# Optimization experiments

Measured on AMD Instinct MI355X. Metric: run time of the kernel, lower is better.

Reference implementation:

```python
import jax, jax.numpy as jnp
import numpy as np

EPS_STAB = 1e-9   # numerical_stabilizer default
BN_EPS = 1e-5     # flax BatchNorm default epsilon


def setup_inputs() -> dict:
    key = jax.random.key(0)
    ks = jax.random.split(key, 5)
    B, N, C = 2, 4096, 512
    s = 1.0 / np.sqrt(C)
    d = {"inputs": jax.random.normal(ks[0], (B, N, C), jnp.float32)}
    # 1x1 convs == pointwise linear maps [C_in, C_out] + bias
    for i, w in enumerate(["Wq", "Wk", "Wv", "Wo"]):
        d[w] = jax.random.normal(ks[1 + i], (C, C), jnp.float32) * s
    for b in ["bq", "bk", "bv", "bo"]:
        d[b] = jnp.zeros((C,), jnp.float32)
    # BatchNorm (inference: use_running_average=True since train=False)
    d["bn_scale"] = jnp.ones((C,), jnp.float32)
    d["bn_bias"] = jnp.zeros((C,), jnp.float32)
    d["bn_mean"] = jnp.zeros((C,), jnp.float32)
    d["bn_var"] = jnp.ones((C,), jnp.float32)
    return d


def reference(inputs, Wq, bq, Wk, bk, Wv, bv, Wo, bo,
              bn_scale, bn_bias, bn_mean, bn_var):
    # QKV via 1x1 conv == dense projection. [B, N, C]
    q = inputs @ Wq + bq
    k = inputs @ Wk + bk
    v = inputs @ Wv + bv
    # scores [B, M, N]; softmax over last axis (N)
    att = jax.nn.softmax(jnp.einsum('bmc,bnc->bmn', q, k), axis=-1)
    # non-standard renorm: divide by column sums (axis=1 == M axis)
    att = att / (EPS_STAB + jnp.sum(att, axis=1, keepdims=True))
    # faithful to einsum '...MN,...NC->...NC': sum attention over M, scale v
    out = v * jnp.sum(att, axis=1)[..., None]
    # output 1x1 conv
    out = out @ Wo + bo
    # BatchNorm with running stats (feature axis -1)
    out = (out - bn_mean) * jax.lax.rsqrt(bn_var + BN_EPS) * bn_scale + bn_bias
    return jax.nn.relu(out) + inputs
```

## Files before the change

kernel.cpp:

```cpp
#include <hip/hip_runtime.h>
#include <hip/hip_bf16.h>

typedef unsigned short u16;
typedef unsigned int u32;
typedef __attribute__((ext_vector_type(8))) short short8;
typedef __attribute__((ext_vector_type(4))) float f32x4;

__device__ __forceinline__ u16 f2bf(float f) {
    union { float f; unsigned u; } v; v.f = f;
    unsigned r = v.u + 0x7fffu + ((v.u >> 16) & 1u);
    return (u16)(r >> 16);
}

__device__ __forceinline__ float fexp2(float x) {
#if __has_builtin(__builtin_amdgcn_exp2f)
    return __builtin_amdgcn_exp2f(x);
#else
    return __expf(x * 0.6931471805599453f);
#endif
}

#if __has_builtin(__builtin_amdgcn_cvt_pk_fp8_f32) && \
    __has_builtin(__builtin_amdgcn_cvt_f32_fp8)
#define FP8_HW 1
#else
#define FP8_HW 0
#endif

#if !FP8_HW
__device__ __forceinline__ u32 sw_fp8(float x) {
    union { float f; u32 u; } v; v.f = x;
    int E = (int)(v.u >> 23) - 127;
    if (x < 0.001953125f) return 0;
    if (E < -6) return (u32)(x * 512.0f + 0.5f);
    u32 m = v.u & 0x7fffffu;
    u32 r = (m + 0x80000u) >> 20;
    u32 bits = ((u32)(E + 7) << 3) + r;
    return bits > 0x7eu ? 0x7eu : bits;
}
__device__ __forceinline__ float sw_fp8d(u32 b) {
    u32 e = (b >> 3) & 15u, m = b & 7u;
    if (e == 0) return (float)m * 0.001953125f;
    union { u32 u; float f; } v; v.u = ((e + 120u) << 23) | (m << 20);
    return v.f;
}
#endif

__device__ __forceinline__ u32 fp8x4_pack(float p0, float p1, float p2, float p3) {
#if FP8_HW
    u32 v = (u32)__builtin_amdgcn_cvt_pk_fp8_f32(p0, p1, 0, false);
    v = (u32)__builtin_amdgcn_cvt_pk_fp8_f32(p2, p3, (int)v, true);
    return v;
#else
    return sw_fp8(p0) | (sw_fp8(p1) << 8) | (sw_fp8(p2) << 16) | (sw_fp8(p3) << 24);
#endif
}

#if FP8_HW
#define FP8_DEC(v, s) __builtin_amdgcn_cvt_f32_fp8((int)(v), (s))
#else
#define FP8_DEC(v, s) sw_fp8d(((v) >> ((s) * 8)) & 0xffu)
#endif

__device__ __forceinline__ void async_cp16(const u16* g, u16* l) {
    __builtin_amdgcn_global_load_lds(
        (const __attribute__((address_space(1))) void*)g,
        (__attribute__((address_space(3))) void*)l, 16, 0, 0);
}

__device__ __forceinline__ short8 mfma_ld(const u16* base, int off) {
    return *(const short8*)&base[off];
}

__device__ __forceinline__ void gemm512(const u16* __restrict__ A,
                                        const u16* __restrict__ B,
                                        u16* As, u16* Bs,
                                        f32x4 acc[4][4], int tid) {
    const int lane = tid & 63, w = tid >> 6;
    const int quad = lane >> 4, l15 = lane & 15;
    const int wm = tid >> 7, wn = (tid >> 6) & 1;
    const int Gw = lane ^ ((lane >> 3) & 7);
    const int srow = Gw >> 3;
    const int scol = (Gw & 7) * 8;
    const int rl = l15 & 7;
    const int winl = l15 >> 3;
    int Pr[2];
#pragma unroll
    for (int h = 0; h < 2; h++)
        Pr[h] = (rl * 8 + ((quad + h * 4) ^ rl)) * 8;
    const int winA0 = (wm * 64) >> 3, winB0 = (wn * 64) >> 3;
    for (int k0 = 0; k0 < 512; k0 += 64) {
        __syncthreads();
#pragma unroll
        for (int t = 0; t < 4; t++) {
            int win = w * 4 + t;
            async_cp16(A + (size_t)(win * 8 + srow) * 512 + k0 + scol,
                       As + win * 512);
            async_cp16(B + (size_t)(win * 8 + srow) * 512 + k0 + scol,
                       Bs + win * 512);
        }
        __syncthreads();
#pragma unroll
        for (int h = 0; h < 2; h++) {
            short8 af[4], bfr[4];
#pragma unroll
            for (int i = 0; i < 4; i++)
                af[i] = mfma_ld(As, (winA0 + i * 2 + winl) * 512 + Pr[h]);
#pragma unroll
            for (int j = 0; j < 4; j++)
                bfr[j] = mfma_ld(Bs, (winB0 + j * 2 + winl) * 512 + Pr[h]);
#pragma unroll
            for (int i = 0; i < 4; i++)
#pragma unroll
                for (int j = 0; j < 4; j++)
                    acc[i][j] = __builtin_amdgcn_mfma_f32_16x16x32_bf16(
                        af[i], bfr[j], acc[i][j], 0, 0, 0);
        }
    }
}

__device__ __forceinline__ void gemm512_r64(const u16* __restrict__ A,
                                            const u16* __restrict__ B,
                                            u16* As, u16* Bs,
                                            f32x4 acc[2][4], int tid) {
    const int lane = tid & 63, w = tid >> 6;
    const int quad = lane >> 4, l15 = lane & 15;
    const int wm = tid >> 7, wn = (tid >> 6) & 1;
    const int Gw = lane ^ ((lane >> 3) & 7);
    const int srow = Gw >> 3;
    const int scol = (Gw & 7) * 8;
    const int rl = l15 & 7;
    const int winl = l15 >> 3;
    int Pr[2];
#pragma unroll
    for (int h = 0; h < 2; h++)
        Pr[h] = (rl * 8 + ((quad + h * 4) ^ rl)) * 8;
    const int winA0 = (wm * 32) >> 3, winB0 = (wn * 64) >> 3;
    for (int k0 = 0; k0 < 512; k0 += 64) {
        __syncthreads();
#pragma unroll
        for (int t = 0; t < 2; t++) {
            int win = w * 2 + t;
            async_cp16(A + (size_t)(win * 8 + srow) * 512 + k0 + scol,
                       As + win * 512);
        }
#pragma unroll
        for (int t = 0; t < 4; t++) {
            int win = w * 4 + t;
            async_cp16(B + (size_t)(win * 8 + srow) * 512 + k0 + scol,
                       Bs + win * 512);
        }
        __syncthreads();
#pragma unroll
        for (int h = 0; h < 2; h++) {
            short8 af[2], bfr[4];
#pragma unroll
            for (int i = 0; i < 2; i++)
                af[i] = mfma_ld(As, (winA0 + i * 2 + winl) * 512 + Pr[h]);
#pragma unroll
            for (int j = 0; j < 4; j++)
                bfr[j] = mfma_ld(Bs, (winB0 + j * 2 + winl) * 512 + Pr[h]);
#pragma unroll
            for (int i = 0; i < 2; i++)
#pragma unroll
                for (int j = 0; j < 4; j++)
                    acc[i][j] = __builtin_amdgcn_mfma_f32_16x16x32_bf16(
                        af[i], bfr[j], acc[i][j], 0, 0, 0);
        }
    }
}

__global__ void prep(const float* __restrict__ X, const float* __restrict__ W0,
                     const float* __restrict__ W1, const float* __restrict__ W2,
                     const float* __restrict__ W3, u16* __restrict__ Xb,
                     u16* __restrict__ T0, u16* __restrict__ T1,
                     u16* __restrict__ T2, u16* __restrict__ T3,
                     float* __restrict__ Sg) {
    __shared__ float tile[32][33];
    int id = blockIdx.x, tid = threadIdx.x;
    if (id == 5120) {
        float4 z = {0.f, 0.f, 0.f, 0.f};
#pragma unroll
        for (int t = 0; t < 8; t++) ((float4*)Sg)[tid + t * 256] = z;
        return;
    }
    if (id < 4096) {
        int idx = (id * 256 + tid) * 4;
        float4 v = *(const float4*)&X[idx];
        ushort4 o;
        o.x = f2bf(v.x); o.y = f2bf(v.y); o.z = f2bf(v.z); o.w = f2bf(v.w);
        *(ushort4*)&Xb[idx] = o;
        return;
    }
    int t = id - 4096;
    int z = t >> 8, rem = t & 255;
    int bo_ = (rem & 15) * 32, bi = (rem >> 4) * 32;
    const float* src; u16* dst;
    switch (z) {
        case 0: src = W0; dst = T0; break;
        case 1: src = W1; dst = T1; break;
        case 2: src = W2; dst = T2; break;
        default: src = W3; dst = T3; break;
    }
    int tx = tid & 31, ty = tid >> 5;
#pragma unroll
    for (int s = 0; s < 4; s++) {
        int i = bi + ty + s * 8;
        tile[ty + s * 8][tx] = src[i * 512 + bo_ + tx];
    }
    __syncthreads();
#pragma unroll
    for (int s = 0; s < 4; s++) {
        int o = bo_ + ty + s * 8;
        dst[o * 512 + bi + tx] = f2bf(tile[tx][ty + s * 8]);
    }
}

__global__ __launch_bounds__(256) void gemm_qkv(
    const u16* __restrict__ Xb, const u16* __restrict__ Wall,
    const float* __restrict__ bq, const float* __restrict__ bk,
    const float* __restrict__ bv, u16* __restrict__ Qall) {
    __shared__ __align__(16) u16 As[8192];
    __shared__ __align__(16) u16 Bs[8192];
    int tid = threadIdx.x;
    int m0 = blockIdx.x * 128, n0 = blockIdx.y * 128, z = blockIdx.z;
    const u16* Bt = Wall + (size_t)z * 262144 + (size_t)n0 * 512;
    const float* bias = (z == 0) ? bq : (z == 1) ? bk : bv;
    const float qs = (z == 0) ? 1.44269504088896340736f : 1.0f;
    u16* C = Qall + (size_t)z * 4194304;
    f32x4 acc[4][4];
#pragma unroll
    for (int i = 0; i < 4; i++)
#pragma unroll
        for (int j = 0; j < 4; j++) acc[i][j] = (f32x4){0.f, 0.f, 0.f, 0.f};
    gemm512(Xb + (size_t)m0 * 512, Bt, As, Bs, acc, tid);
    int lane = tid & 63, quad = lane >> 4, l15 = lane & 15;
    int wm = tid >> 7, wn = (tid >> 6) & 1;
#pragma unroll
    for (int j = 0; j < 4; j++) {
        int n = n0 + wn * 64 + j * 16 + l15;
        float bvv = bias[n];
#pragma unroll
        for (int i = 0; i < 4; i++)
#pragma unroll
            for (int rg = 0; rg < 4; rg++) {
                int m = m0 + wm * 64 + i * 16 + quad * 4 + rg;
                C[(size_t)m * 512 + n] = f2bf((acc[i][j][rg] + bvv) * qs);
            }
    }
}

__global__ __launch_bounds__(256) void attn_pass1p(
    const u16* __restrict__ Qb, const u16* __restrict__ Kb,
    float2* __restrict__ statsP, u32* __restrict__ Pbuf) {
    __shared__ __align__(16) u16 As[8192];
    __shared__ __align__(16) u16 Bs[8192];
    int tid = threadIdx.x;
    int mblk = blockIdx.x, nch = blockIdx.y, b = blockIdx.z;
    const u16* Q = Qb + ((size_t)(b * 4096 + mblk * 128)) * 512;
    int lane = tid & 63, quad = lane >> 4, l15 = lane & 15;
    int wm = tid >> 7, wn = (tid >> 6) & 1;
    for (int nt = 0; nt < 2; nt++) {
        const u16* K = Kb + ((size_t)(b * 4096 + nch * 256 + nt * 128)) * 512;
        f32x4 acc[4][4];
#pragma unroll
        for (int i = 0; i < 4; i++)
#pragma unroll
            for (int j = 0; j < 4; j++) acc[i][j] = (f32x4){0.f, 0.f, 0.f, 0.f};
        gemm512(Q, K, As, Bs, acc, tid);
        u32* Pt = Pbuf + (((size_t)(b * 32 + mblk) * 16 + nch) * 2 + nt) * 4096;
        int ch = nch * 4 + nt * 2 + wn;
#pragma unroll
        for (int i = 0; i < 4; i++)
#pragma unroll
            for (int rg = 0; rg < 4; rg++) {
                float v0 = acc[i][0][rg], v1 = acc[i][1][rg];
                float v2 = acc[i][2][rg], v3 = acc[i][3][rg];
                float Mt = fmaxf(fmaxf(v0, v1), fmaxf(v2, v3));
                Mt = fmaxf(Mt, __shfl_xor(Mt, 1));
                Mt = fmaxf(Mt, __shfl_xor(Mt, 2));
                Mt = fmaxf(Mt, __shfl_xor(Mt, 4));
                Mt = fmaxf(Mt, __shfl_xor(Mt, 8));
                float e8 = Mt - 8.0f;
                float p0 = fexp2(v0 - e8), p1 = fexp2(v1 - e8);
                float p2 = fexp2(v2 - e8), p3 = fexp2(v3 - e8);
                Pt[(i * 4 + rg) * 256 + tid] = fp8x4_pack(p0, p1, p2, p3);
                float L = p0 + p1 + p2 + p3;
                L += __shfl_xor(L, 1);
                L += __shfl_xor(L, 2);
                L += __shfl_xor(L, 4);
                L += __shfl_xor(L, 8);
                if (l15 == 0)
                    statsP[((size_t)(b * 64 + ch)) * 4096 + mblk * 128 +
                           wm * 64 + i * 16 + quad * 4 + rg] =
                        make_float2(Mt, L * 0.00390625f);
            }
    }
}

__global__ void reduce_stats2(const float2* __restrict__ statsP,
                              float* __restrict__ cstat) {
    int t = blockIdx.x * 256 + threadIdx.x;
    int b = t >> 12, m = t & 4095;
    const float2* sp = statsP + (size_t)b * 64 * 4096 + m;
    float M = -INFINITY;
#pragma unroll 4
    for (int ch = 0; ch < 64; ch++) M = fmaxf(M, sp[(size_t)ch * 4096].x);
    float Z = 0.f;
#pragma unroll 4
    for (int ch = 0; ch < 64; ch++) {
        float2 p = sp[(size_t)ch * 4096];
        Z += p.y * fexp2(p.x - M);
    }
    cstat[t] = M + __log2f(Z);
}

__global__ __launch_bounds__(256) void colsum(
    const u32* __restrict__ Pbuf, const float2* __restrict__ statsP,
    const float* __restrict__ cstat, float* __restrict__ Sg) {
    int tid = threadIdx.x, lane = tid & 63;
    int wm = tid >> 7, wn = (tid >> 6) & 1, quad = lane >> 4;
    int nch = blockIdx.x, nt = blockIdx.y & 1, mgrp = blockIdx.y >> 1;
    int b = blockIdx.z;
    int ch = nch * 4 + nt * 2 + wn;
    const float2* Sp = statsP + ((size_t)(b * 64 + ch)) * 4096;
    const float* Cp = cstat + (size_t)b * 4096;
    float cp[4] = {0.f, 0.f, 0.f, 0.f};
    for (int mb = 0; mb < 2; mb++) {
        int mblk = mgrp * 2 + mb;
        const u32* Pt =
            Pbuf + (((size_t)(b * 32 + mblk) * 16 + nch) * 2 + nt) * 4096;
#pragma unroll
        for (int i = 0; i < 4; i++) {
            int r0 = mblk * 128 + wm * 64 + i * 16 + quad * 4;
            float4 s01 = *(const float4*)&Sp[r0];
            float4 s23 = *(const float4*)&Sp[r0 + 2];
            float4 cv = *(const float4*)&Cp[r0];
            float fv[4] = {fexp2(s01.x - 8.0f - cv.x),
                           fexp2(s01.z - 8.0f - cv.y),
                           fexp2(s23.x - 8.0f - cv.z),
                           fexp2(s23.z - 8.0f - cv.w)};
            float fm = fmaxf(fmaxf(fv[0], fv[1]), fmaxf(fv[2], fv[3]));
            if (fm > 3.469446951953614e-18f) {
#pragma unroll
                for (int rg = 0; rg < 4; rg++) {
                    u32 e = Pt[(i * 4 + rg) * 256 + tid];
                    cp[0] += FP8_DEC(e, 0) * fv[rg];
                    cp[1] += FP8_DEC(e, 1) * fv[rg];
                    cp[2] += FP8_DEC(e, 2) * fv[rg];
                    cp[3] += FP8_DEC(e, 3) * fv[rg];
                }
            }
        }
    }
#pragma unroll
    for (int j = 0; j < 4; j++) {
        float s = cp[j];
        s += __shfl_xor(s, 16);
        s += __shfl_xor(s, 32);
        if (lane < 16)
            atomicAdd(&Sg[b * 4096 + nch * 256 + nt * 128 + wn * 64 + j * 16 + lane], s);
    }
}

__global__ __launch_bounds__(256) void gemm_final(
    const u16* __restrict__ A, const u16* __restrict__ Bt,
    const float* __restrict__ Sg, const float* __restrict__ bo,
    const float* __restrict__ g, const float* __restrict__ bb,
    const float* __restrict__ mean, const float* __restrict__ var,
    const float* __restrict__ X, float* __restrict__ out) {
    __shared__ __align__(16) u16 As[4096];
    __shared__ __align__(16) u16 Bs[8192];
    int tid = threadIdx.x;
    int m0 = blockIdx.x * 64, n0 = blockIdx.y * 128;
    f32x4 acc[2][4];
#pragma unroll
    for (int i = 0; i < 2; i++)
#pragma unroll
        for (int j = 0; j < 4; j++) acc[i][j] = (f32x4){0.f, 0.f, 0.f, 0.f};
    gemm512_r64(A + (size_t)m0 * 512, Bt + (size_t)n0 * 512, As, Bs, acc, tid);
    int lane = tid & 63, quad = lane >> 4, l15 = lane & 15;
    int wm = tid >> 7, wn = (tid >> 6) & 1;
    float sc[2][4];
#pragma unroll
    for (int i = 0; i < 2; i++) {
        float4 s = *(const float4*)&Sg[m0 + wm * 32 + i * 16 + quad * 4];
        float v[4] = {s.x, s.y, s.z, s.w};
#pragma unroll
        for (int rg = 0; rg < 4; rg++) sc[i][rg] = v[rg] / (1e-9f + v[rg]);
    }
#pragma unroll
    for (int j = 0; j < 4; j++) {
        int n = n0 + wn * 64 + j * 16 + l15;
        float aj = rsqrtf(var[n] + 1e-5f) * g[n];
        float cj = bb[n] - mean[n] * aj;
        float bj = bo[n];
#pragma unroll
        for (int i = 0; i < 2; i++)
#pragma unroll
            for (int rg = 0; rg < 4; rg++) {
                int m = m0 + wm * 32 + i * 16 + quad * 4 + rg;
                float x = acc[i][j][rg] * sc[i][rg] + bj;
                float y = x * aj + cj;
                out[(size_t)m * 512 + n] = fmaxf(y, 0.f) + X[(size_t)m * 512 + n];
            }
    }
}

extern "C" void kernel_launch(void* const* d_in, const int* in_sizes, int n_in,
                              void* d_out, int out_size, void* d_ws, size_t ws_size,
                              hipStream_t stream) {
    const float* X  = (const float*)d_in[0];
    const float* Wq = (const float*)d_in[1];
    const float* Wk = (const float*)d_in[2];
    const float* Wv = (const float*)d_in[3];
    const float* Wo = (const float*)d_in[4];
    const float* bq = (const float*)d_in[5];
    const float* bk = (const float*)d_in[6];
    const float* bv = (const float*)d_in[7];
    const float* bo = (const float*)d_in[8];
    const float* g    = (const float*)d_in[9];
    const float* bb   = (const float*)d_in[10];
    const float* mean = (const float*)d_in[11];
    const float* var  = (const float*)d_in[12];
    float* out = (float*)d_out;

    char* ws = (char*)d_ws;
    u16* Xb  = (u16*)(ws + 0);
    u16* Wqt = (u16*)(ws + 8388608);
    u16* Wot = (u16*)(ws + 9961472);
    u16* Qb  = (u16*)(ws + 10485760);
    u16* Kb  = (u16*)(ws + 18874368);
    u16* Vb  = (u16*)(ws + 27262976);
    float2* statsP = (float2*)(ws + 35651584);
    float* Sg      = (float*)(ws + 39845888);
    float* cstat   = (float*)(ws + 39878656);
    u32* Pbuf      = (u32*)(ws + 39911424);

    prep<<<5121, 256, 0, stream>>>(X, Wq, Wk, Wv, Wo, Xb, Wqt, Wqt + 262144,
                                   Wqt + 524288, Wot, Sg);
    gemm_qkv<<<dim3(64, 4, 3), 256, 0, stream>>>(Xb, Wqt, bq, bk, bv, Qb);
    attn_pass1p<<<dim3(32, 16, 2), 256, 0, stream>>>(Qb, Kb, statsP, Pbuf);
    reduce_stats2<<<32, 256, 0, stream>>>(statsP, cstat);
    colsum<<<dim3(16, 32, 2), 256, 0, stream>>>(Pbuf, statsP, cstat, Sg);
    gemm_final<<<dim3(128, 4), 256, 0, stream>>>(Vb, Wot, Sg, bo, g, bb, mean, var,
                                                 X, out);
}
```

Measured before the change: 216.7 us.

## Fuse QKV, attention, stats, colsum and output GEMM into one persistent kernel

Replaces five separate launches with a single persistent kernel of 1024 blocks that runs each stage in turn, separated by software grid barriers built on atomic counters. The counters are zeroed in prep. The stats reduction is reworked to use warp-shuffle merging, with 32 lanes per row. The aim is to remove launch gaps and kernel-boundary drains between stages. In exchange it depends on all 1024 blocks being co-resident (launch_bounds 256,4 on 256 CUs), and spin-waiting plus load imbalance across phases can add stall time.

```diff
diff --git a/kernel.cpp b/kernel.cpp
--- a/kernel.cpp
+++ b/kernel.cpp
@@ -72,8 +72,7 @@
     return *(const short8*)&base[off];
 }
 
-__device__ __forceinline__ void gemm512(const u16* __restrict__ A,
-                                        const u16* __restrict__ B,
+__device__ __forceinline__ void gemm512(const u16* A, const u16* B,
                                         u16* As, u16* Bs,
                                         f32x4 acc[4][4], int tid) {
     const int lane = tid & 63, w = tid >> 6;
@@ -119,8 +118,7 @@
     }
 }
 
-__device__ __forceinline__ void gemm512_r64(const u16* __restrict__ A,
-                                            const u16* __restrict__ B,
+__device__ __forceinline__ void gemm512_r64(const u16* A, const u16* B,
                                             u16* As, u16* Bs,
                                             f32x4 acc[2][4], int tid) {
     const int lane = tid & 63, w = tid >> 6;
@@ -170,18 +168,33 @@
     }
 }
 
+__device__ __forceinline__ void gridbar(u32* ctr, u32 target, int tid) {
+    __syncthreads();
+    __threadfence();
+    if (tid == 0) {
+        __hip_atomic_fetch_add(ctr, 1u, __ATOMIC_ACQ_REL,
+                               __HIP_MEMORY_SCOPE_AGENT);
+        int it = 0;
+        while (__hip_atomic_load(ctr, __ATOMIC_ACQUIRE,
+                                 __HIP_MEMORY_SCOPE_AGENT) < target &&
+               it < (1 << 24)) {
+            __builtin_amdgcn_s_sleep(2);
+            ++it;
+        }
+    }
+    __syncthreads();
+}
+
 __global__ void prep(const float* __restrict__ X, const float* __restrict__ W0,
                      const float* __restrict__ W1, const float* __restrict__ W2,
                      const float* __restrict__ W3, u16* __restrict__ Xb,
                      u16* __restrict__ T0, u16* __restrict__ T1,
                      u16* __restrict__ T2, u16* __restrict__ T3,
-                     float* __restrict__ Sg) {
+                     u32* __restrict__ ctr) {
     __shared__ float tile[32][33];
     int id = blockIdx.x, tid = threadIdx.x;
     if (id == 5120) {
-        float4 z = {0.f, 0.f, 0.f, 0.f};
-#pragma unroll
-        for (int t = 0; t < 8; t++) ((float4*)Sg)[tid + t * 256] = z;
+        if (tid < 4) ctr[tid] = 0;
         return;
     }
     if (id < 4096) {
@@ -216,194 +229,199 @@
     }
 }
 
-__global__ __launch_bounds__(256) void gemm_qkv(
-    const u16* __restrict__ Xb, const u16* __restrict__ Wall,
-    const float* __restrict__ bq, const float* __restrict__ bk,
-    const float* __restrict__ bv, u16* __restrict__ Qall) {
-    __shared__ __align__(16) u16 As[8192];
-    __shared__ __align__(16) u16 Bs[8192];
-    int tid = threadIdx.x;
-    int m0 = blockIdx.x * 128, n0 = blockIdx.y * 128, z = blockIdx.z;
-    const u16* Bt = Wall + (size_t)z * 262144 + (size_t)n0 * 512;
-    const float* bias = (z == 0) ? bq : (z == 1) ? bk : bv;
-    const float qs = (z == 0) ? 1.44269504088896340736f : 1.0f;
-    u16* C = Qall + (size_t)z * 4194304;
-    f32x4 acc[4][4];
-#pragma unroll
-    for (int i = 0; i < 4; i++)
-#pragma unroll
-        for (int j = 0; j < 4; j++) acc[i][j] = (f32x4){0.f, 0.f, 0.f, 0.f};
-    gemm512(Xb + (size_t)m0 * 512, Bt, As, Bs, acc, tid);
+__global__ __launch_bounds__(256, 4) void mega(
+    const u16* Xb, const u16* Wall, const float* bq, const float* bk,
+    const float* bv, u16* Qall, float2* statsP, u32* Pbuf, float* cstat,
+    float* Sg, const u16* Wot, const float* bo, const float* g,
+    const float* bb, const float* mean, const float* var, const float* X,
+    float* out, u32* ctr) {
+    __shared__ __align__(16) u16 LDS[16384];
+    u16* As = LDS;
+    u16* Bs = LDS + 8192;
+    int tid = threadIdx.x, bid = blockIdx.x;
     int lane = tid & 63, quad = lane >> 4, l15 = lane & 15;
     int wm = tid >> 7, wn = (tid >> 6) & 1;
-#pragma unroll
-    for (int j = 0; j < 4; j++) {
-        int n = n0 + wn * 64 + j * 16 + l15;
-        float bvv = bias[n];
+
+    if (bid < 768) {
+        int z = bid >> 8, rem = bid & 255;
+        int m0 = (rem >> 2) * 128, n0 = (rem & 3) * 128;
+        const u16* Bt = Wall + (size_t)z * 262144 + (size_t)n0 * 512;
+        const float* bias = (z == 0) ? bq : (z == 1) ? bk : bv;
+        const float qs = (z == 0) ? 1.44269504088896340736f : 1.0f;
+        u16* C = Qall + (size_t)z * 4194304;
+        f32x4 acc[4][4];
 #pragma unroll
         for (int i = 0; i < 4; i++)
 #pragma unroll
-            for (int rg = 0; rg < 4; rg++) {
-                int m = m0 + wm * 64 + i * 16 + quad * 4 + rg;
-                C[(size_t)m * 512 + n] = f2bf((acc[i][j][rg] + bvv) * qs);
-            }
-    }
-}
-
-__global__ __launch_bounds__(256) void attn_pass1p(
-    const u16* __restrict__ Qb, const u16* __restrict__ Kb,
-    float2* __restrict__ statsP, u32* __restrict__ Pbuf) {
-    __shared__ __align__(16) u16 As[8192];
-    __shared__ __align__(16) u16 Bs[8192];
-    int tid = threadIdx.x;
-    int mblk = blockIdx.x, nch = blockIdx.y, b = blockIdx.z;
-    const u16* Q = Qb + ((size_t)(b * 4096 + mblk * 128)) * 512;
-    int lane = tid & 63, quad = lane >> 4, l15 = lane & 15;
-    int wm = tid >> 7, wn = (tid >> 6) & 1;
-    for (int nt = 0; nt < 2; nt++) {
-        const u16* K = Kb + ((size_t)(b * 4096 + nch * 256 + nt * 128)) * 512;
-        f32x4 acc[4][4];
-#pragma unroll
-        for (int i = 0; i < 4; i++)
-#pragma unroll
             for (int j = 0; j < 4; j++) acc[i][j] = (f32x4){0.f, 0.f, 0.f, 0.f};
-        gemm512(Q, K, As, Bs, acc, tid);
-        u32* Pt = Pbuf + (((size_t)(b * 32 + mblk) * 16 + nch) * 2 + nt) * 4096;
+        gemm512(Xb + (size_t)m0 * 512, Bt, As, Bs, acc, tid);
+#pragma unroll
+        for (int j = 0; j < 4; j++) {
+            int n = n0 + wn * 64 + j * 16 + l15;
+            float bvv = bias[n];
+#pragma unroll
+            for (int i = 0; i < 4; i++)
+#pragma unroll
+                for (int rg = 0; rg < 4; rg++) {
+                    int m = m0 + wm * 64 + i * 16 + quad * 4 + rg;
+                    C[(size_t)m * 512 + n] = f2bf((acc[i][j][rg] + bvv) * qs);
+                }
+        }
+    }
+    gridbar(ctr + 0, 1024, tid);
+
+    {
+        int mblk = bid & 31, nch = (bid >> 5) & 15, b = bid >> 9;
+        const u16* Qp = Qall + ((size_t)(b * 4096 + mblk * 128)) * 512;
+        const u16* Kbase = Qall + 4194304;
+        for (int nt = 0; nt < 2; nt++) {
+            const u16* K =
+                Kbase + ((size_t)(b * 4096 + nch * 256 + nt * 128)) * 512;
+            f32x4 acc[4][4];
+#pragma unroll
+            for (int i = 0; i < 4; i++)
+#pragma unroll
+                for (int j = 0; j < 4; j++)
+                    acc[i][j] = (f32x4){0.f, 0.f, 0.f, 0.f};
+            gemm512(Qp, K, As, Bs, acc, tid);
+            u32* Pt =
+                Pbuf + (((size_t)(b * 32 + mblk) * 16 + nch) * 2 + nt) * 4096;
+            int ch = nch * 4 + nt * 2 + wn;
+#pragma unroll
+            for (int i = 0; i < 4; i++)
+#pragma unroll
+                for (int rg = 0; rg < 4; rg++) {
+                    float v0 = acc[i][0][rg], v1 = acc[i][1][rg];
+                    float v2 = acc[i][2][rg], v3 = acc[i][3][rg];
+                    float Mt = fmaxf(fmaxf(v0, v1), fmaxf(v2, v3));
+                    Mt = fmaxf(Mt, __shfl_xor(Mt, 1));
+                    Mt = fmaxf(Mt, __shfl_xor(Mt, 2));
+                    Mt = fmaxf(Mt, __shfl_xor(Mt, 4));
+                    Mt = fmaxf(Mt, __shfl_xor(Mt, 8));
+                    float e8 = Mt - 8.0f;
+                    float p0 = fexp2(v0 - e8), p1 = fexp2(v1 - e8);
+                    float p2 = fexp2(v2 - e8), p3 = fexp2(v3 - e8);
+                    Pt[(i * 4 + rg) * 256 + tid] = fp8x4_pack(p0, p1, p2, p3);
+                    float L = p0 + p1 + p2 + p3;
+                    L += __shfl_xor(L, 1);
+                    L += __shfl_xor(L, 2);
+                    L += __shfl_xor(L, 4);
+                    L += __shfl_xor(L, 8);
+                    if (l15 == 0)
+                        statsP[((size_t)(b * 64 + ch)) * 4096 + mblk * 128 +
+                               wm * 64 + i * 16 + quad * 4 + rg] =
+                            make_float2(Mt, L * 0.00390625f);
+                }
+        }
+    }
+    gridbar(ctr + 1, 1024, tid);
+
+    {
+        int row = bid * 8 + (tid >> 5);
+        int q = tid & 31;
+        int b = row >> 12, m = row & 4095;
+        const float2* sp = statsP + (size_t)b * 64 * 4096 + m;
+        float2 pa = sp[(size_t)(q * 2) * 4096];
+        float2 pb = sp[(size_t)(q * 2 + 1) * 4096];
+        float M = fmaxf(pa.x, pb.x);
+        float Z = pa.y * fexp2(pa.x - M) + pb.y * fexp2(pb.x - M);
+#pragma unroll
+        for (int d = 1; d < 32; d <<= 1) {
+            float Mo = __shfl_xor(M, d);
+            float Zo = __shfl_xor(Z, d);
+            float Mn = fmaxf(M, Mo);
+            Z = Z * fexp2(M - Mn) + Zo * fexp2(Mo - Mn);
+            M = Mn;
+        }
+        if (q == 0) {
+            cstat[row] = M + __log2f(Z);
+            Sg[row] = 0.f;
+        }
+    }
+    gridbar(ctr + 2, 1024, tid);
+
+    {
+        int nch = bid & 15, y = (bid >> 4) & 31, b = bid >> 9;
+        int nt = y & 1, mgrp = y >> 1;
         int ch = nch * 4 + nt * 2 + wn;
-#pragma unroll
-        for (int i = 0; i < 4; i++)
-#pragma unroll
-            for (int rg = 0; rg < 4; rg++) {
-                float v0 = acc[i][0][rg], v1 = acc[i][1][rg];
-                float v2 = acc[i][2][rg], v3 = acc[i][3][rg];
-                float Mt = fmaxf(fmaxf(v0, v1), fmaxf(v2, v3));
-                Mt = fmaxf(Mt, __shfl_xor(Mt, 1));
-                Mt = fmaxf(Mt, __shfl_xor(Mt, 2));
-                Mt = fmaxf(Mt, __shfl_xor(Mt, 4));
-                Mt = fmaxf(Mt, __shfl_xor(Mt, 8));
-                float e8 = Mt - 8.0f;
-                float p0 = fexp2(v0 - e8), p1 = fexp2(v1 - e8);
-                float p2 = fexp2(v2 - e8), p3 = fexp2(v3 - e8);
-                Pt[(i * 4 + rg) * 256 + tid] = fp8x4_pack(p0, p1, p2, p3);
-                float L = p0 + p1 + p2 + p3;
-                L += __shfl_xor(L, 1);
-                L += __shfl_xor(L, 2);
-                L += __shfl_xor(L, 4);
-                L += __shfl_xor(L, 8);
-                if (l15 == 0)
-                    statsP[((size_t)(b * 64 + ch)) * 4096 + mblk * 128 +
-                           wm * 64 + i * 16 + quad * 4 + rg] =
-                        make_float2(Mt, L * 0.00390625f);
-            }
-    }
-}
-
-__global__ void reduce_stats2(const float2* __restrict__ statsP,
-                              float* __restrict__ cstat) {
-    int t = blockIdx.x * 256 + threadIdx.x;
-    int b = t >> 12, m = t & 4095;
-    const float2* sp = statsP + (size_t)b * 64 * 4096 + m;
-    float M = -INFINITY;
-#pragma unroll 4
-    for (int ch = 0; ch < 64; ch++) M = fmaxf(M, sp[(size_t)ch * 4096].x);
-    float Z = 0.f;
-#pragma unroll 4
-    for (int ch = 0; ch < 64; ch++) {
-        float2 p = sp[(size_t)ch * 4096];
-        Z += p.y * fexp2(p.x - M);
-    }
-    cstat[t] = M + __log2f(Z);
-}
-
-__global__ __launch_bounds__(256) void colsum(
-    const u32* __restrict__ Pbuf, const float2* __restrict__ statsP,
-    const float* __restrict__ cstat, float* __restrict__ Sg) {
-    int tid = threadIdx.x, lane = tid & 63;
-    int wm = tid >> 7, wn = (tid >> 6) & 1, quad = lane >> 4;
-    int nch = blockIdx.x, nt = blockIdx.y & 1, mgrp = blockIdx.y >> 1;
-    int b = blockIdx.z;
-    int ch = nch * 4 + nt * 2 + wn;
-    const float2* Sp = statsP + ((size_t)(b * 64 + ch)) * 4096;
-    const float* Cp = cstat + (size_t)b * 4096;
-    float cp[4] = {0.f, 0.f, 0.f, 0.f};
-    for (int mb = 0; mb < 2; mb++) {
-        int mblk = mgrp * 2 + mb;
-        const u32* Pt =
-            Pbuf + (((size_t)(b * 32 + mblk) * 16 + nch) * 2 + nt) * 4096;
-#pragma unroll
-        for (int i = 0; i < 4; i++) {
-            int r0 = mblk * 128 + wm * 64 + i * 16 + quad * 4;
-            float4 s01 = *(const float4*)&Sp[r0];
-            float4 s23 = *(const float4*)&Sp[r0 + 2];
-            float4 cv = *(const float4*)&Cp[r0];
-            float fv[4] = {fexp2(s01.x - 8.0f - cv.x),
-                           fexp2(s01.z - 8.0f - cv.y),
-                           fexp2(s23.x - 8.0f - cv.z),
-                           fexp2(s23.z - 8.0f - cv.w)};
-            float fm = fmaxf(fmaxf(fv[0], fv[1]), fmaxf(fv[2], fv[3]));
-            if (fm > 3.469446951953614e-18f) {
-#pragma unroll
-                for (int rg = 0; rg < 4; rg++) {
-                    u32 e = Pt[(i * 4 + rg) * 256 + tid];
-                    cp[0] += FP8_DEC(e, 0) * fv[rg];
-                    cp[1] += FP8_DEC(e, 1) * fv[rg];
-                    cp[2] += FP8_DEC(e, 2) * fv[rg];
-                    cp[3] += FP8_DEC(e, 3) * fv[rg];
+        const float2* Sp = statsP + ((size_t)(b * 64 + ch)) * 4096;
+        const float* Cp = cstat + (size_t)b * 4096;
+        float cp[4] = {0.f, 0.f, 0.f, 0.f};
+        for (int mb = 0; mb < 2; mb++) {
+            int mblk = mgrp * 2 + mb;
+            const u32* Pt =
+                Pbuf + (((size_t)(b * 32 + mblk) * 16 + nch) * 2 + nt) * 4096;
+#pragma unroll
+            for (int i = 0; i < 4; i++) {
+                int r0 = mblk * 128 + wm * 64 + i * 16 + quad * 4;
+                float4 s01 = *(const float4*)&Sp[r0];
+                float4 s23 = *(const float4*)&Sp[r0 + 2];
+                float4 cv = *(const float4*)&Cp[r0];
+                float fv[4] = {fexp2(s01.x - 8.0f - cv.x),
+                               fexp2(s01.z - 8.0f - cv.y),
+                               fexp2(s23.x - 8.0f - cv.z),
+                               fexp2(s23.z - 8.0f - cv.w)};
+                float fm = fmaxf(fmaxf(fv[0], fv[1]), fmaxf(fv[2], fv[3]));
+                if (fm > 3.469446951953614e-18f) {
+#pragma unroll
+                    for (int rg = 0; rg < 4; rg++) {
+                        u32 e = Pt[(i * 4 + rg) * 256 + tid];
+                        cp[0] += FP8_DEC(e, 0) * fv[rg];
+                        cp[1] += FP8_DEC(e, 1) * fv[rg];
+                        cp[2] += FP8_DEC(e, 2) * fv[rg];
+                        cp[3] += FP8_DEC(e, 3) * fv[rg];
+                    }
                 }
             }
         }
-    }
-#pragma unroll
-    for (int j = 0; j < 4; j++) {
-        float s = cp[j];
-        s += __shfl_xor(s, 16);
-        s += __shfl_xor(s, 32);
-        if (lane < 16)
-            atomicAdd(&Sg[b * 4096 + nch * 256 + nt * 128 + wn * 64 + j * 16 + lane], s);
-    }
-}
-
-__global__ __launch_bounds__(256) void gemm_final(
-    const u16* __restrict__ A, const u16* __restrict__ Bt,
-    const float* __restrict__ Sg, const float* __restrict__ bo,
-    const float* __restrict__ g, const float* __restrict__ bb,
-    const float* __restrict__ mean, const float* __restrict__ var,
-    const float* __restrict__ X, float* __restrict__ out) {
-    __shared__ __align__(16) u16 As[4096];
-    __shared__ __align__(16) u16 Bs[8192];
-    int tid = threadIdx.x;
-    int m0 = blockIdx.x * 64, n0 = blockIdx.y * 128;
-    f32x4 acc[2][4];
-#pragma unroll
-    for (int i = 0; i < 2; i++)
-#pragma unroll
-        for (int j = 0; j < 4; j++) acc[i][j] = (f32x4){0.f, 0.f, 0.f, 0.f};
-    gemm512_r64(A + (size_t)m0 * 512, Bt + (size_t)n0 * 512, As, Bs, acc, tid);
-    int lane = tid & 63, quad = lane >> 4, l15 = lane & 15;
-    int wm = tid >> 7, wn = (tid >> 6) & 1;
-    float sc[2][4];
-#pragma unroll
-    for (int i = 0; i < 2; i++) {
-        float4 s = *(const float4*)&Sg[m0 + wm * 32 + i * 16 + quad * 4];
-        float v[4] = {s.x, s.y, s.z, s.w};
-#pragma unroll
-        for (int rg = 0; rg < 4; rg++) sc[i][rg] = v[rg] / (1e-9f + v[rg]);
-    }
-#pragma unroll
-    for (int j = 0; j < 4; j++) {
-        int n = n0 + wn * 64 + j * 16 + l15;
-        float aj = rsqrtf(var[n] + 1e-5f) * g[n];
-        float cj = bb[n] - mean[n] * aj;
-        float bj = bo[n];
+#pragma unroll
+        for (int j = 0; j < 4; j++) {
+            float s = cp[j];
+            s += __shfl_xor(s, 16);
+            s += __shfl_xor(s, 32);
+            if (lane < 16)
+                atomicAdd(&Sg[b * 4096 + nch * 256 + nt * 128 + wn * 64 +
+                              j * 16 + lane],
+                          s);
+        }
+    }
+    gridbar(ctr + 3, 1024, tid);
+
+    if (bid < 512) {
+        int m0 = (bid & 127) * 64, n0 = (bid >> 7) * 128;
+        const u16* Vb = Qall + 2 * 4194304;
+        f32x4 acc[2][4];
 #pragma unroll
         for (int i = 0; i < 2; i++)
 #pragma unroll
-            for (int rg = 0; rg < 4; rg++) {
-                int m = m0 + wm * 32 + i * 16 + quad * 4 + rg;
-                float x = acc[i][j][rg] * sc[i][rg] + bj;
-                float y = x * aj + cj;
-                out[(size_t)m * 512 + n] = fmaxf(y, 0.f) + X[(size_t)m * 512 + n];
-            }
+            for (int j = 0; j < 4; j++) acc[i][j] = (f32x4){0.f, 0.f, 0.f, 0.f};
+        gemm512_r64(Vb + (size_t)m0 * 512, Wot + (size_t)n0 * 512, LDS,
+                    LDS + 4096, acc, tid);
+        float sc[2][4];
+#pragma unroll
+        for (int i = 0; i < 2; i++) {
+            float4 s = *(const float4*)&Sg[m0 + wm * 32 + i * 16 + quad * 4];
+            float v[4] = {s.x, s.y, s.z, s.w};
+#pragma unroll
+            for (int rg = 0; rg < 4; rg++) sc[i][rg] = v[rg] / (1e-9f + v[rg]);
+        }
+#pragma unroll
+        for (int j = 0; j < 4; j++) {
+            int n = n0 + wn * 64 + j * 16 + l15;
+            float aj = rsqrtf(var[n] + 1e-5f) * g[n];
+            float cj = bb[n] - mean[n] * aj;
+            float bj = bo[n];
+#pragma unroll
+            for (int i = 0; i < 2; i++)
+#pragma unroll
+                for (int rg = 0; rg < 4; rg++) {
+                    int m = m0 + wm * 32 + i * 16 + quad * 4 + rg;
+                    float x = acc[i][j][rg] * sc[i][rg] + bj;
+                    float y = x * aj + cj;
+                    out[(size_t)m * 512 + n] =
+                        fmaxf(y, 0.f) + X[(size_t)m * 512 + n];
+                }
+        }
     }
 }
 
@@ -430,19 +448,15 @@
     u16* Wqt = (u16*)(ws + 8388608);
     u16* Wot = (u16*)(ws + 9961472);
     u16* Qb  = (u16*)(ws + 10485760);
-    u16* Kb  = (u16*)(ws + 18874368);
-    u16* Vb  = (u16*)(ws + 27262976);
     float2* statsP = (float2*)(ws + 35651584);
     float* Sg      = (float*)(ws + 39845888);
     float* cstat   = (float*)(ws + 39878656);
-    u32* Pbuf      = (u32*)(ws + 39911424);
+    u32* ctr       = (u32*)(ws + 39911424);
+    u32* Pbuf      = (u32*)(ws + 39911680);
 
     prep<<<5121, 256, 0, stream>>>(X, Wq, Wk, Wv, Wo, Xb, Wqt, Wqt + 262144,
-                                   Wqt + 524288, Wot, Sg);
-    gemm_qkv<<<dim3(64, 4, 3), 256, 0, stream>>>(Xb, Wqt, bq, bk, bv, Qb);
-    attn_pass1p<<<dim3(32, 16, 2), 256, 0, stream>>>(Qb, Kb, statsP, Pbuf);
-    reduce_stats2<<<32, 256, 0, stream>>>(statsP, cstat);
-    colsum<<<dim3(16, 32, 2), 256, 0, stream>>>(Pbuf, statsP, cstat, Sg);
-    gemm_final<<<dim3(128, 4), 256, 0, stream>>>(Vb, Wot, Sg, bo, g, bb, mean, var,
-                                                 X, out);
-}
+                                   Wqt + 524288, Wot, ctr);
+    mega<<<1024, 256, 0, stream>>>(Xb, Wqt, bq, bk, bv, Qb, statsP, Pbuf,
+                                   cstat, Sg, Wot, bo, g, bb, mean, var, X,
+                                   out, ctr);
+}
```

Result: slower. 856.3 us (+295.2%).
